# Kernel tuning notes

Hardware: AMD Instinct MI355X
Metric: run time of the kernel (lower is better)

The kernel has to match this reference:

```python
import jax, jax.numpy as jnp
import numpy as np

B, T, D, H = 4, 4096, 1024, 64

def setup_inputs() -> dict:
    key = jax.random.key(0)
    k1, k2, k3, k4 = jax.random.split(key, 4)
    scale = 1.0 / np.sqrt(D)
    return {
        "x": jax.random.normal(k1, (B, T, D), dtype=jnp.float32),
        "Wq": jax.random.normal(k2, (D, H), dtype=jnp.float32) * scale,
        "Wk": jax.random.normal(k3, (D, H), dtype=jnp.float32) * scale,
        "Wv": jax.random.normal(k4, (D, H), dtype=jnp.float32) * scale,
    }

def reference(x, Wq, Wk, Wv):
    # Projections (Linear without bias): [B,T,H]
    q = jnp.einsum('btd,dh->bth', x, Wq)
    k = jnp.einsum('btd,dh->bth', x, Wk)
    v = jnp.einsum('btd,dh->bth', x, Wv)
    head_size = q.shape[-1]
    # Full T x T scores, scaled by sqrt(head_size) as in the source
    attn = jnp.einsum('bqh,bkh->bqk', q, k) / jnp.sqrt(jnp.float32(head_size))
    t = x.shape[1]
    causal = jnp.tril(jnp.ones((t, t), dtype=bool))  # [T,T]
    attn = jnp.where(causal[None, :, :], attn, -jnp.inf)
    attn = jax.nn.softmax(attn, axis=-1)
    # dropout prob = 0.0 -> identity
    out = jnp.einsum('bqk,bkh->bqh', attn, v)
    return out
```

## Files before the change

kernel.cpp:

```cpp
#include <hip/hip_runtime.h>
#include <hip/hip_bf16.h>
#include <math.h>

#define BB 4
#define TT 4096
#define DD 1024
#define HH 64
#define MTOT (BB * TT)
#define LD 72
#define NCH 4

typedef short short8 __attribute__((ext_vector_type(8)));
typedef float f32x4  __attribute__((ext_vector_type(4)));
typedef unsigned int u32;

__device__ __forceinline__ unsigned short f2bf(float f) {
    unsigned u = __builtin_bit_cast(unsigned, f);
    unsigned r = (u + 0x7fffu + ((u >> 16) & 1u)) >> 16;
    return (unsigned short)r;
}

__device__ __forceinline__ unsigned long long pack4(float a, float b, float c, float d) {
    return (unsigned long long)f2bf(a) |
           ((unsigned long long)f2bf(b) << 16) |
           ((unsigned long long)f2bf(c) << 32) |
           ((unsigned long long)f2bf(d) << 48);
}

__device__ __forceinline__ short8 pack8(float4 a, float4 b) {
    short8 r;
    r[0] = (short)f2bf(a.x); r[1] = (short)f2bf(a.y);
    r[2] = (short)f2bf(a.z); r[3] = (short)f2bf(a.w);
    r[4] = (short)f2bf(b.x); r[5] = (short)f2bf(b.y);
    r[6] = (short)f2bf(b.z); r[7] = (short)f2bf(b.w);
    return r;
}

__device__ __forceinline__ void gl16(const void* g, void* l) {
    __builtin_amdgcn_global_load_lds(
        (const __attribute__((address_space(1))) u32*)g,
        (__attribute__((address_space(3))) u32*)l, 16, 0, 0);
}

#define QOFF  0
#define KOFF  (MTOT * HH)
#define VOFF  (2 * MTOT * HH)
#define BF_TOTAL (3 * MTOT * HH)

__global__ __launch_bounds__(256) void transpose_w(
    const float* __restrict__ Wq, const float* __restrict__ Wk,
    const float* __restrict__ Wv, unsigned short* __restrict__ Wt)
{
    const int w = blockIdx.y;
    const float* W = (w == 0) ? Wq : (w == 1) ? Wk : Wv;
    unsigned short* o = Wt + (size_t)w * 64 * 1024;
    const int t  = threadIdx.x;
    const int n4 = t & 15;
    const int k0 = blockIdx.x * 64 + (t >> 4) * 4;

    float v[4][4];
#pragma unroll
    for (int ii = 0; ii < 4; ++ii) {
        float4 r = *(const float4*)&W[(size_t)(k0 + ii) * HH + n4 * 4];
        v[ii][0] = r.x; v[ii][1] = r.y; v[ii][2] = r.z; v[ii][3] = r.w;
    }
#pragma unroll
    for (int cc = 0; cc < 4; ++cc) {
        unsigned long long pk = pack4(v[0][cc], v[1][cc], v[2][cc], v[3][cc]);
        *(unsigned long long*)&o[(size_t)(n4 * 4 + cc) * 1024 + k0] = pk;
    }
}

__global__ __launch_bounds__(256, 2) void qkv_proj(
    const float* __restrict__ x,
    const unsigned short* __restrict__ Wt,
    unsigned short* __restrict__ qkv)
{
    const int tid   = threadIdx.x;
    const int lane  = tid & 63;
    const int wave  = tid >> 6;
    const int l15   = lane & 15;
    const int quad  = lane >> 4;
    const int m0    = blockIdx.x * 32;
    const int strip = wave & 1;
    const int half  = wave >> 1;

    __shared__ float          Af[2][32 * 64];
    __shared__ unsigned short Bs[2][192 * 64];

    const int ar  = lane >> 4;
    const int as  = lane & 15;
    const int bc  = lane >> 3;
    const int bs2 = (lane & 7) ^ bc;

#define STAGE(it, p)                                                         \
    {                                                                        \
        const int kc_ = (it) * 64;                                           \
        _Pragma("unroll")                                                    \
        for (int jj = 0; jj < 2; ++jj) {                                     \
            int j   = wave * 2 + jj;                                         \
            int row = 4 * j + ar;                                            \
            int sw  = as ^ (row & 15);                                       \
            gl16(x + (size_t)(m0 + row) * DD + kc_ + sw * 4,                 \
                 &Af[p][j * 256]);                                           \
        }                                                                    \
        _Pragma("unroll")                                                    \
        for (int jj = 0; jj < 6; ++jj) {                                     \
            int j    = wave * 6 + jj;                                        \
            int gcol = 8 * j + bc;                                           \
            gl16(Wt + (size_t)gcol * 1024 + kc_ + bs2 * 8,                   \
                 &Bs[p][j * 512]);                                           \
        }                                                                    \
    }

    f32x4 acc[6];
#pragma unroll
    for (int i = 0; i < 6; ++i) acc[i] = (f32x4){0.f, 0.f, 0.f, 0.f};

    STAGE(0, 0)
    __syncthreads();
    int p = 0;

    for (int it = 0; it < 16; ++it) {
        if (it < 15) STAGE(it + 1, p ^ 1)

        const int row = strip * 16 + l15;
#pragma unroll
        for (int ks = 0; ks < 2; ++ks) {
            int c0 = ks * 8 + quad * 2;
            float4 a0 = *(const float4*)&Af[p][row * 64 + ((c0)     ^ l15) * 4];
            float4 a1 = *(const float4*)&Af[p][row * 64 + ((c0 + 1) ^ l15) * 4];
            short8 af = pack8(a0, a1);
            int cb = (ks * 4 + quad) ^ (l15 & 7);
#pragma unroll
            for (int jj = 0; jj < 6; ++jj) {
                int col = (half * 6 + jj) * 16 + l15;
                short8 bfr = *(const short8*)&Bs[p][col * 64 + cb * 8];
                acc[jj] = __builtin_amdgcn_mfma_f32_16x16x32_bf16(af, bfr, acc[jj], 0, 0, 0);
            }
        }
        __syncthreads();
        p ^= 1;
    }
#undef STAGE

    unsigned short* q_bf  = qkv + QOFF;
    unsigned short* k_bf  = qkv + KOFF;
    unsigned short* vt_bf = qkv + VOFF;
#pragma unroll
    for (int jj = 0; jj < 6; ++jj) {
        int g = half * 6 + jj, w = g >> 2, col = (g & 3) * 16 + l15;
#pragma unroll
        for (int r = 0; r < 4; ++r) {
            int m = m0 + strip * 16 + quad * 4 + r;
            unsigned short bv = f2bf(acc[jj][r]);
            if (w == 0)      q_bf[(size_t)m * HH + col] = bv;
            else if (w == 1) k_bf[(size_t)m * HH + col] = bv;
            else {
                int b = m >> 12, t = m & 4095;
                vt_bf[(size_t)b * HH * TT + (size_t)col * TT + t] = bv;
            }
        }
    }
}

__global__ __launch_bounds__(256) void flash_attn(
    const unsigned short* __restrict__ qkv,
    float* __restrict__ Opart,
    float* __restrict__ Mpart,
    float* __restrict__ Lpart)
{
    const int qt = 63 - blockIdx.x;
    const int b  = blockIdx.y;
    const int c  = blockIdx.z;
    if (c * 16 > qt) return;
    const int j0   = c * 16;
    const int jmax = min(j0 + 16, qt + 1);

    const int tid  = threadIdx.x;
    const int lane = tid & 63;
    const int wave = tid >> 6;
    const int l15  = lane & 15;
    const int quad = lane >> 4;

    const unsigned short* q_g  = qkv + QOFF + (size_t)b * TT * HH;
    const unsigned short* k_g  = qkv + KOFF + (size_t)b * TT * HH;
    const unsigned short* vt_g = qkv + VOFF + (size_t)b * HH * TT;

    __shared__ unsigned short Ks[128 * LD];
    __shared__ unsigned short Vs[64 * 136];
    __shared__ unsigned short Ps[4 * 16 * LD];
    unsigned short* Pw = Ps + wave * 16 * LD;

    short8 qf[2];
#pragma unroll
    for (int kk = 0; kk < 2; ++kk)
        qf[kk] = *(const short8*)&q_g[(size_t)(qt * 64 + wave * 16 + l15) * HH + kk * 32 + quad * 8];

    f32x4 ov[4];
#pragma unroll
    for (int i = 0; i < 4; ++i) ov[i] = (f32x4){0.f, 0.f, 0.f, 0.f};
    float m_run = -1e30f, l_run = 0.f;

    const int srow = tid >> 3;
    const int seg  = tid & 7;

    const float SC = 0.125f * 1.44269504088896f;

    for (int jr = j0; jr < jmax; jr += 2) {
        const int nrow = min(jmax - jr, 2) * 64;
        __syncthreads();

#pragma unroll
        for (int r4 = 0; r4 < 4; ++r4) {
            int row = srow + r4 * 32;
            if (row < nrow)
                *(ulonglong2*)&Ks[row * LD + seg * 8] =
                    *(const ulonglong2*)&k_g[(size_t)(jr * 64 + row) * HH + seg * 8];
        }
#pragma unroll
        for (int c2 = 0; c2 < 2; ++c2) {
            int chunk = seg + c2 * 8;
            if (chunk * 8 < nrow) {
#pragma unroll
                for (int r2 = 0; r2 < 2; ++r2) {
                    int h = srow + r2 * 32;
                    *(ulonglong2*)&Vs[h * 136 + chunk * 8] =
                        *(const ulonglong2*)&vt_g[(size_t)h * TT + jr * 64 + chunk * 8];
                }
            }
        }
        __syncthreads();

        const int jend = min(jr + 2, jmax);
        for (int j = jr; j < jend; ++j) {
            const int tl = (j - jr) * 64;

            f32x4 st[4];
#pragma unroll
            for (int i = 0; i < 4; ++i) st[i] = (f32x4){0.f, 0.f, 0.f, 0.f};
#pragma unroll
            for (int kk = 0; kk < 2; ++kk)
#pragma unroll
                for (int mt = 0; mt < 4; ++mt) {
                    short8 a = *(const short8*)&Ks[(tl + mt * 16 + l15) * LD + kk * 32 + quad * 8];
                    st[mt] = __builtin_amdgcn_mfma_f32_16x16x32_bf16(a, qf[kk], st[mt], 0, 0, 0);
                }

#pragma unroll
            for (int mt = 0; mt < 4; ++mt)
#pragma unroll
                for (int r = 0; r < 4; ++r) st[mt][r] *= SC;
            if (j == qt) {
                int qg = wave * 16 + l15;
#pragma unroll
                for (int mt = 0; mt < 4; ++mt)
#pragma unroll
                    for (int r = 0; r < 4; ++r)
                        if (mt * 16 + quad * 4 + r > qg) st[mt][r] = -1e30f;
            }

            float mloc = -1e30f;
#pragma unroll
            for (int mt = 0; mt < 4; ++mt)
#pragma unroll
                for (int r = 0; r < 4; ++r) mloc = fmaxf(mloc, st[mt][r]);
            mloc = fmaxf(mloc, __shfl_xor(mloc, 16));
            mloc = fmaxf(mloc, __shfl_xor(mloc, 32));
            float m_new = fmaxf(m_run, mloc);
            float alpha = exp2f(m_run - m_new);
            m_run = m_new;

            float ssum = 0.f;
#pragma unroll
            for (int mt = 0; mt < 4; ++mt)
#pragma unroll
                for (int r = 0; r < 4; ++r) {
                    float p = exp2f(st[mt][r] - m_new);
                    st[mt][r] = p;
                    ssum += p;
                }
            ssum += __shfl_xor(ssum, 16);
            ssum += __shfl_xor(ssum, 32);
            l_run = l_run * alpha + ssum;

#pragma unroll
            for (int mt = 0; mt < 4; ++mt)
                *(unsigned long long*)&Pw[l15 * LD + mt * 16 + quad * 4] =
                    pack4(st[mt][0], st[mt][1], st[mt][2], st[mt][3]);

            float a4[4];
#pragma unroll
            for (int r = 0; r < 4; ++r) a4[r] = __shfl(alpha, quad * 4 + r);
#pragma unroll
            for (int ht = 0; ht < 4; ++ht)
#pragma unroll
                for (int r = 0; r < 4; ++r) ov[ht][r] *= a4[r];

#pragma unroll
            for (int kk = 0; kk < 2; ++kk) {
                short8 a = *(const short8*)&Pw[l15 * LD + kk * 32 + quad * 8];
#pragma unroll
                for (int ht = 0; ht < 4; ++ht) {
                    short8 bf = *(const short8*)&Vs[(ht * 16 + l15) * 136 + tl + kk * 32 + quad * 8];
                    ov[ht] = __builtin_amdgcn_mfma_f32_16x16x32_bf16(a, bf, ov[ht], 0, 0, 0);
                }
            }
        }
    }

    float* Ob = Opart + ((size_t)((b * 64 + qt) * NCH + c)) * 4096;
#pragma unroll
    for (int ht = 0; ht < 4; ++ht)
#pragma unroll
        for (int r = 0; r < 4; ++r)
            Ob[(size_t)(wave * 16 + quad * 4 + r) * HH + ht * 16 + l15] = ov[ht][r];
    if (quad == 0) {
        size_t mi = (size_t)((b * 64 + qt) * NCH + c) * 64 + wave * 16 + l15;
        Mpart[mi] = m_run;
        Lpart[mi] = l_run;
    }
}

__global__ __launch_bounds__(256) void combine(
    const float* __restrict__ Opart,
    const float* __restrict__ Mpart,
    const float* __restrict__ Lpart,
    float* __restrict__ out)
{
    const int qt = blockIdx.x;
    const int b  = blockIdx.y;
    const int nc = (qt >> 4) + 1;
    const int t  = threadIdx.x;
    const int row = t >> 2;
    const int seg = t & 3;

    const size_t base = (size_t)(b * 64 + qt) * NCH;

    float m_c[NCH], M = -1e30f;
    for (int c = 0; c < nc; ++c) {
        m_c[c] = Mpart[(base + c) * 64 + row];
        M = fmaxf(M, m_c[c]);
    }
    float L = 0.f, w_c[NCH];
    for (int c = 0; c < nc; ++c) {
        w_c[c] = exp2f(m_c[c] - M);
        L += w_c[c] * Lpart[(base + c) * 64 + row];
    }
    float invL = 1.0f / L;

    f32x4 o[4];
#pragma unroll
    for (int i = 0; i < 4; ++i) o[i] = (f32x4){0.f, 0.f, 0.f, 0.f};
    for (int c = 0; c < nc; ++c) {
        const float* Ob = Opart + (base + c) * 4096 + (size_t)row * HH + seg * 16;
#pragma unroll
        for (int i = 0; i < 4; ++i) {
            f32x4 v = *(const f32x4*)(Ob + i * 4);
            o[i] += v * w_c[c];
        }
    }
    float* op = out + ((size_t)b * TT + qt * 64 + row) * HH + seg * 16;
#pragma unroll
    for (int i = 0; i < 4; ++i)
        *(f32x4*)(op + i * 4) = o[i] * invL;
}

extern "C" void kernel_launch(void* const* d_in, const int* in_sizes, int n_in,
                              void* d_out, int out_size, void* d_ws, size_t ws_size,
                              hipStream_t stream) {
    const float* x  = (const float*)d_in[0];
    const float* Wq = (const float*)d_in[1];
    const float* Wk = (const float*)d_in[2];
    const float* Wv = (const float*)d_in[3];
    float* out = (float*)d_out;

    unsigned short* qkv = (unsigned short*)d_ws;
    float* Opart = (float*)((char*)d_ws + BF_TOTAL * 2);
    float* Mpart = Opart + (size_t)BB * 64 * NCH * 4096;
    float* Lpart = Mpart + (size_t)BB * 64 * NCH * 64;

    unsigned short* Wt = (unsigned short*)d_out;

    transpose_w<<<dim3(16, 3), 256, 0, stream>>>(Wq, Wk, Wv, Wt);
    qkv_proj<<<dim3(MTOT / 32), 256, 0, stream>>>(x, Wt, qkv);
    flash_attn<<<dim3(64, BB, NCH), 256, 0, stream>>>(qkv, Opart, Mpart, Lpart);
    combine<<<dim3(64, BB), 256, 0, stream>>>(Opart, Mpart, Lpart, out);
}
```

Baseline: 167.4 us.

## Load K/V fragments directly from global, fold softmax scale into Q, process two tiles jointly

Removes the shared-memory staging of K and V tiles and the block-wide barriers. Each wave now loads its MFMA fragments straight from global memory and runs one online-softmax update over 128 keys instead of two updates over 64. The softmax scale is folded into Q at projection time, the probabilities are packed with the hardware bf16 convert instruction, and the blocks are remapped so batches and chunks interleave, with launch bounds set for two blocks per SM. The cost is redundant global/L2 traffic, since the four waves each fetch the same K/V data, and higher register pressure from holding two score tiles and V fragments.

Result: slower. 207.3 us (+23.8%).

```diff
diff --git a/kernel.cpp b/kernel.cpp
--- a/kernel.cpp
+++ b/kernel.cpp
@@ -7,8 +7,8 @@
 #define DD 1024
 #define HH 64
 #define MTOT (BB * TT)
-#define LD 72
 #define NCH 4
+#define LDP 136
 
 typedef short short8 __attribute__((ext_vector_type(8)));
 typedef float f32x4  __attribute__((ext_vector_type(4)));
@@ -144,6 +144,7 @@
     }
 #undef STAGE
 
+    const float QS = 0.125f * 1.44269504088896f;
     unsigned short* q_bf  = qkv + QOFF;
     unsigned short* k_bf  = qkv + KOFF;
     unsigned short* vt_bf = qkv + VOFF;
@@ -153,7 +154,9 @@
 #pragma unroll
         for (int r = 0; r < 4; ++r) {
             int m = m0 + strip * 16 + quad * 4 + r;
-            unsigned short bv = f2bf(acc[jj][r]);
+            float val = acc[jj][r];
+            if (w == 0) val *= QS;
+            unsigned short bv = f2bf(val);
             if (w == 0)      q_bf[(size_t)m * HH + col] = bv;
             else if (w == 1) k_bf[(size_t)m * HH + col] = bv;
             else {
@@ -164,15 +167,17 @@
     }
 }
 
-__global__ __launch_bounds__(256) void flash_attn(
+__global__ __launch_bounds__(256, 2) void flash_attn(
     const unsigned short* __restrict__ qkv,
     float* __restrict__ Opart,
     float* __restrict__ Mpart,
     float* __restrict__ Lpart)
 {
-    const int qt = 63 - blockIdx.x;
-    const int b  = blockIdx.y;
-    const int c  = blockIdx.z;
+    const int id   = blockIdx.x + (blockIdx.y << 6) + (blockIdx.z << 8);
+    const int b    = (id & 7) >> 1;
+    const int rest = id >> 3;
+    const int qt   = 63 - (rest & 63);
+    const int c    = ((rest >> 6) << 1) | (id & 1);
     if (c * 16 > qt) return;
     const int j0   = c * 16;
     const int jmax = min(j0 + 16, qt + 1);
@@ -187,10 +192,8 @@
     const unsigned short* k_g  = qkv + KOFF + (size_t)b * TT * HH;
     const unsigned short* vt_g = qkv + VOFF + (size_t)b * HH * TT;
 
-    __shared__ unsigned short Ks[128 * LD];
-    __shared__ unsigned short Vs[64 * 136];
-    __shared__ unsigned short Ps[4 * 16 * LD];
-    unsigned short* Pw = Ps + wave * 16 * LD;
+    __shared__ unsigned short Ps[4 * 16 * LDP];
+    unsigned short* Pw = Ps + wave * 16 * LDP;
 
     short8 qf[2];
 #pragma unroll
@@ -202,109 +205,145 @@
     for (int i = 0; i < 4; ++i) ov[i] = (f32x4){0.f, 0.f, 0.f, 0.f};
     float m_run = -1e30f, l_run = 0.f;
 
-    const int srow = tid >> 3;
-    const int seg  = tid & 7;
-
-    const float SC = 0.125f * 1.44269504088896f;
-
     for (int jr = j0; jr < jmax; jr += 2) {
-        const int nrow = min(jmax - jr, 2) * 64;
-        __syncthreads();
-
-#pragma unroll
-        for (int r4 = 0; r4 < 4; ++r4) {
-            int row = srow + r4 * 32;
-            if (row < nrow)
-                *(ulonglong2*)&Ks[row * LD + seg * 8] =
-                    *(const ulonglong2*)&k_g[(size_t)(jr * 64 + row) * HH + seg * 8];
-        }
-#pragma unroll
-        for (int c2 = 0; c2 < 2; ++c2) {
-            int chunk = seg + c2 * 8;
-            if (chunk * 8 < nrow) {
-#pragma unroll
-                for (int r2 = 0; r2 < 2; ++r2) {
-                    int h = srow + r2 * 32;
-                    *(ulonglong2*)&Vs[h * 136 + chunk * 8] =
-                        *(const ulonglong2*)&vt_g[(size_t)h * TT + jr * 64 + chunk * 8];
+        const bool two = (jmax - jr) >= 2;
+        const unsigned short* kr = k_g  + (size_t)jr * 64 * HH;
+        const unsigned short* vr = vt_g + (size_t)jr * 64;
+
+        f32x4 st0[4], st1[4];
+#pragma unroll
+        for (int i = 0; i < 4; ++i) {
+            st0[i] = (f32x4){0.f, 0.f, 0.f, 0.f};
+            st1[i] = (f32x4){0.f, 0.f, 0.f, 0.f};
+        }
+#pragma unroll
+        for (int kk = 0; kk < 2; ++kk)
+#pragma unroll
+            for (int mt = 0; mt < 4; ++mt) {
+                short8 a = *(const short8*)&kr[(size_t)(mt * 16 + l15) * HH + kk * 32 + quad * 8];
+                st0[mt] = __builtin_amdgcn_mfma_f32_16x16x32_bf16(a, qf[kk], st0[mt], 0, 0, 0);
+            }
+        if (two) {
+#pragma unroll
+            for (int kk = 0; kk < 2; ++kk)
+#pragma unroll
+                for (int mt = 0; mt < 4; ++mt) {
+                    short8 a = *(const short8*)&kr[(size_t)(64 + mt * 16 + l15) * HH + kk * 32 + quad * 8];
+                    st1[mt] = __builtin_amdgcn_mfma_f32_16x16x32_bf16(a, qf[kk], st1[mt], 0, 0, 0);
                 }
-            }
-        }
-        __syncthreads();
-
-        const int jend = min(jr + 2, jmax);
-        for (int j = jr; j < jend; ++j) {
-            const int tl = (j - jr) * 64;
-
-            f32x4 st[4];
-#pragma unroll
-            for (int i = 0; i < 4; ++i) st[i] = (f32x4){0.f, 0.f, 0.f, 0.f};
+        }
+
+        short8 vf0[8], vf1[8];
+#pragma unroll
+        for (int kk = 0; kk < 2; ++kk)
+#pragma unroll
+            for (int ht = 0; ht < 4; ++ht)
+                vf0[kk * 4 + ht] = *(const short8*)&vr[(size_t)(ht * 16 + l15) * TT + kk * 32 + quad * 8];
+        if (two) {
 #pragma unroll
             for (int kk = 0; kk < 2; ++kk)
 #pragma unroll
-                for (int mt = 0; mt < 4; ++mt) {
-                    short8 a = *(const short8*)&Ks[(tl + mt * 16 + l15) * LD + kk * 32 + quad * 8];
-                    st[mt] = __builtin_amdgcn_mfma_f32_16x16x32_bf16(a, qf[kk], st[mt], 0, 0, 0);
+                for (int ht = 0; ht < 4; ++ht)
+                    vf1[kk * 4 + ht] = *(const short8*)&vr[(size_t)(ht * 16 + l15) * TT + 64 + kk * 32 + quad * 8];
+        }
+
+        const int qg = wave * 16 + l15;
+        if (jr == qt) {
+#pragma unroll
+            for (int mt = 0; mt < 4; ++mt)
+#pragma unroll
+                for (int r = 0; r < 4; ++r)
+                    if (mt * 16 + quad * 4 + r > qg) st0[mt][r] = -1e30f;
+        } else if (two && jr + 1 == qt) {
+#pragma unroll
+            for (int mt = 0; mt < 4; ++mt)
+#pragma unroll
+                for (int r = 0; r < 4; ++r)
+                    if (mt * 16 + quad * 4 + r > qg) st1[mt][r] = -1e30f;
+        }
+
+        float mloc = -1e30f;
+#pragma unroll
+        for (int mt = 0; mt < 4; ++mt)
+#pragma unroll
+            for (int r = 0; r < 4; ++r) mloc = fmaxf(mloc, st0[mt][r]);
+        if (two) {
+#pragma unroll
+            for (int mt = 0; mt < 4; ++mt)
+#pragma unroll
+                for (int r = 0; r < 4; ++r) mloc = fmaxf(mloc, st1[mt][r]);
+        }
+        mloc = fmaxf(mloc, __shfl_xor(mloc, 16));
+        mloc = fmaxf(mloc, __shfl_xor(mloc, 32));
+        const float m_new = fmaxf(m_run, mloc);
+        const float alpha = exp2f(m_run - m_new);
+        m_run = m_new;
+
+        float ssum = 0.f;
+#pragma unroll
+        for (int mt = 0; mt < 4; ++mt)
+#pragma unroll
+            for (int r = 0; r < 4; ++r) {
+                float pv = exp2f(st0[mt][r] - m_new);
+                st0[mt][r] = pv; ssum += pv;
+            }
+        if (two) {
+#pragma unroll
+            for (int mt = 0; mt < 4; ++mt)
+#pragma unroll
+                for (int r = 0; r < 4; ++r) {
+                    float pv = exp2f(st1[mt][r] - m_new);
+                    st1[mt][r] = pv; ssum += pv;
                 }
-
-#pragma unroll
-            for (int mt = 0; mt < 4; ++mt)
-#pragma unroll
-                for (int r = 0; r < 4; ++r) st[mt][r] *= SC;
-            if (j == qt) {
-                int qg = wave * 16 + l15;
-#pragma unroll
-                for (int mt = 0; mt < 4; ++mt)
-#pragma unroll
-                    for (int r = 0; r < 4; ++r)
-                        if (mt * 16 + quad * 4 + r > qg) st[mt][r] = -1e30f;
-            }
-
-            float mloc = -1e30f;
-#pragma unroll
-            for (int mt = 0; mt < 4; ++mt)
-#pragma unroll
-                for (int r = 0; r < 4; ++r) mloc = fmaxf(mloc, st[mt][r]);
-            mloc = fmaxf(mloc, __shfl_xor(mloc, 16));
-            mloc = fmaxf(mloc, __shfl_xor(mloc, 32));
-            float m_new = fmaxf(m_run, mloc);
-            float alpha = exp2f(m_run - m_new);
-            m_run = m_new;
-
-            float ssum = 0.f;
-#pragma unroll
-            for (int mt = 0; mt < 4; ++mt)
-#pragma unroll
-                for (int r = 0; r < 4; ++r) {
-                    float p = exp2f(st[mt][r] - m_new);
-                    st[mt][r] = p;
-                    ssum += p;
-                }
-            ssum += __shfl_xor(ssum, 16);
-            ssum += __shfl_xor(ssum, 32);
-            l_run = l_run * alpha + ssum;
-
-#pragma unroll
-            for (int mt = 0; mt < 4; ++mt)
-                *(unsigned long long*)&Pw[l15 * LD + mt * 16 + quad * 4] =
-                    pack4(st[mt][0], st[mt][1], st[mt][2], st[mt][3]);
-
-            float a4[4];
-#pragma unroll
-            for (int r = 0; r < 4; ++r) a4[r] = __shfl(alpha, quad * 4 + r);
+        }
+        ssum += __shfl_xor(ssum, 16);
+        ssum += __shfl_xor(ssum, 32);
+        l_run = l_run * alpha + ssum;
+
+#pragma unroll
+        for (int mt = 0; mt < 4; ++mt) {
+            u32 p0, p1;
+            asm("v_cvt_pk_bf16_f32 %0, %1, %2" : "=v"(p0) : "v"(st0[mt][0]), "v"(st0[mt][1]));
+            asm("v_cvt_pk_bf16_f32 %0, %1, %2" : "=v"(p1) : "v"(st0[mt][2]), "v"(st0[mt][3]));
+            uint2 pr; pr.x = p0; pr.y = p1;
+            *(uint2*)&Pw[l15 * LDP + mt * 16 + quad * 4] = pr;
+        }
+        if (two) {
+#pragma unroll
+            for (int mt = 0; mt < 4; ++mt) {
+                u32 p0, p1;
+                asm("v_cvt_pk_bf16_f32 %0, %1, %2" : "=v"(p0) : "v"(st1[mt][0]), "v"(st1[mt][1]));
+                asm("v_cvt_pk_bf16_f32 %0, %1, %2" : "=v"(p1) : "v"(st1[mt][2]), "v"(st1[mt][3]));
+                uint2 pr; pr.x = p0; pr.y = p1;
+                *(uint2*)&Pw[l15 * LDP + 64 + mt * 16 + quad * 4] = pr;
+            }
+        }
+
+        {
+            float a0 = __shfl(alpha, quad * 4 + 0);
+            float a1 = __shfl(alpha, quad * 4 + 1);
+            float a2 = __shfl(alpha, quad * 4 + 2);
+            float a3 = __shfl(alpha, quad * 4 + 3);
+#pragma unroll
+            for (int ht = 0; ht < 4; ++ht) {
+                ov[ht][0] *= a0; ov[ht][1] *= a1;
+                ov[ht][2] *= a2; ov[ht][3] *= a3;
+            }
+        }
+#pragma unroll
+        for (int kk = 0; kk < 2; ++kk) {
+            short8 a = *(const short8*)&Pw[l15 * LDP + kk * 32 + quad * 8];
 #pragma unroll
             for (int ht = 0; ht < 4; ++ht)
-#pragma unroll
-                for (int r = 0; r < 4; ++r) ov[ht][r] *= a4[r];
-
+                ov[ht] = __builtin_amdgcn_mfma_f32_16x16x32_bf16(a, vf0[kk * 4 + ht], ov[ht], 0, 0, 0);
+        }
+        if (two) {
 #pragma unroll
             for (int kk = 0; kk < 2; ++kk) {
-                short8 a = *(const short8*)&Pw[l15 * LD + kk * 32 + quad * 8];
-#pragma unroll
-                for (int ht = 0; ht < 4; ++ht) {
-                    short8 bf = *(const short8*)&Vs[(ht * 16 + l15) * 136 + tl + kk * 32 + quad * 8];
-                    ov[ht] = __builtin_amdgcn_mfma_f32_16x16x32_bf16(a, bf, ov[ht], 0, 0, 0);
-                }
+                short8 a = *(const short8*)&Pw[l15 * LDP + 64 + kk * 32 + quad * 8];
+#pragma unroll
+                for (int ht = 0; ht < 4; ++ht)
+                    ov[ht] = __builtin_amdgcn_mfma_f32_16x16x32_bf16(a, vf1[kk * 4 + ht], ov[ht], 0, 0, 0);
             }
         }
     }
```
